# Performance work log

Hardware: AMD Instinct MI355X
Metric: run time of the kernel (lower is better)

## Reference

```python
import jax, jax.numpy as jnp
import numpy as np

D_MODEL = 2048
N_HEADS = 16
HEAD_DIM = D_MODEL // N_HEADS  # 128
B, T = 2, 2048


def setup_inputs() -> dict:
    key = jax.random.key(0)
    ks = jax.random.split(key, 9)
    s = 0.02
    x = jax.random.normal(ks[0], (B, T, D_MODEL), dtype=jnp.float32)
    # Per-head projection weights (stacked over heads); torch Linear y = x @ W^T + b,
    # here W is stored as [H, d_model, head_dim] so y = einsum('btc,hcd->bhtd').
    Wq = jax.random.normal(ks[1], (N_HEADS, D_MODEL, HEAD_DIM), dtype=jnp.float32) * s
    bq = jax.random.normal(ks[2], (N_HEADS, HEAD_DIM), dtype=jnp.float32) * s
    Wk = jax.random.normal(ks[3], (N_HEADS, D_MODEL, HEAD_DIM), dtype=jnp.float32) * s
    bk = jax.random.normal(ks[4], (N_HEADS, HEAD_DIM), dtype=jnp.float32) * s
    Wv = jax.random.normal(ks[5], (N_HEADS, D_MODEL, HEAD_DIM), dtype=jnp.float32) * s
    bv = jax.random.normal(ks[6], (N_HEADS, HEAD_DIM), dtype=jnp.float32) * s
    Wo = jax.random.normal(ks[7], (D_MODEL, D_MODEL), dtype=jnp.float32) * s  # used as y @ Wo
    bo = jax.random.normal(ks[8], (D_MODEL,), dtype=jnp.float32) * s
    return {"x": x, "Wq": Wq, "bq": bq, "Wk": Wk, "bk": bk,
            "Wv": Wv, "bv": bv, "Wo": Wo, "bo": bo}


def reference(x, Wq, bq, Wk, bk, Wv, bv, Wo, bo):
    # x: [B, T, C]; per-head Q/K/V projections -> [B, H, T, D]
    Bn, Tn, C = x.shape
    H, _, D = Wq.shape
    scale = D ** (-0.5)
    q = jnp.einsum('btc,hcd->bhtd', x, Wq) + bq[None, :, None, :]
    k = jnp.einsum('btc,hcd->bhtd', x, Wk) + bk[None, :, None, :]
    v = jnp.einsum('btc,hcd->bhtd', x, Wv) + bv[None, :, None, :]
    # scores [B, H, T, T] with additive causal mask (finfo.min above the diagonal)
    scores = jnp.einsum('bhtd,bhsd->bhts', q, k) * scale
    neg = jnp.finfo(scores.dtype).min
    causal = jnp.triu(jnp.full((Tn, Tn), neg, dtype=scores.dtype), k=1)
    probs = jax.nn.softmax(scores + causal, axis=-1)
    y = jnp.einsum('bhts,bhsd->bhtd', probs, v)  # [B, H, T, D]
    # concat heads along feature dim (head order preserved) then output projection
    y = y.transpose(0, 2, 1, 3).reshape(Bn, Tn, H * D)
    return y @ Wo + bo
```

## Files before the change

kernel.cpp:

```cpp
#include <hip/hip_runtime.h>
#include <stdint.h>

typedef unsigned short u16;
typedef __attribute__((ext_vector_type(4))) u16 u16x4;
typedef __attribute__((ext_vector_type(8))) u16 u16x8;
typedef __attribute__((ext_vector_type(8))) __bf16 bf16x8;
typedef __attribute__((ext_vector_type(4))) float f32x4;
typedef __attribute__((ext_vector_type(16))) float f32x16;

#define D_MODEL 2048
#define N_HEADS 16
#define HEAD_DIM 128
#define BATCH 2
#define SEQ 2048
#define M_TOT (BATCH*SEQ)
#define N_QKV (3*D_MODEL)

__device__ __forceinline__ u16 f2b(float f) {
  union { float f; uint32_t u; } c; c.f = f;
  uint32_t u = c.u;
  uint32_t r = (u + 0x7fffu + ((u >> 16) & 1u)) >> 16;
  return (u16)r;
}

__device__ __forceinline__ void gl_lds16(const u16* g, u16* l) {
  __builtin_amdgcn_global_load_lds(
      (const __attribute__((address_space(1))) uint32_t*)g,
      (__attribute__((address_space(3))) uint32_t*)l, 16, 0, 0);
}

template <int N> __device__ __forceinline__ void waitvm() {
  if constexpr (N == 6)      asm volatile("s_waitcnt vmcnt(6)" ::: "memory");
  else if constexpr (N == 5) asm volatile("s_waitcnt vmcnt(5)" ::: "memory");
  else                       asm volatile("s_waitcnt vmcnt(0)" ::: "memory");
}

__global__ __launch_bounds__(256) void prep_kernel(
    const float* __restrict__ x, u16* __restrict__ xb,
    const float* __restrict__ Wq, const float* __restrict__ Wk,
    const float* __restrict__ Wv, u16* __restrict__ Wt) {
  __shared__ u16 Tl[128][72];
  const int bid = blockIdx.x, tid = threadIdx.x;
  if (bid < 8192) {
    int i = (bid * 256 + tid) * 4;
    f32x4 v = *(const f32x4*)(x + i);
    u16x4 o;
    o[0] = f2b(v[0]); o[1] = f2b(v[1]); o[2] = f2b(v[2]); o[3] = f2b(v[3]);
    *(u16x4*)(xb + i) = o;
    return;
  }
  const int rel = bid - 8192;
  const int k0 = (rel & 31) * 64;
  const int hh = rel >> 5;
  const int qkv = hh >> 4, h = hh & 15;
  const float* src = (qkv == 0 ? Wq : qkv == 1 ? Wk : Wv) + (size_t)h * 2048 * 128;
  for (int it = 0; it < 32; ++it) {
    int idx = it * 256 + tid;
    int k = idx >> 7, d = idx & 127;
    Tl[d][k] = f2b(src[(size_t)(k0 + k) * 128 + d]);
  }
  __syncthreads();
  for (int it = 0; it < 32; ++it) {
    int idx = it * 256 + tid;
    int d = idx >> 6, kk = idx & 63;
    Wt[(size_t)(hh * 128 + d) * 2048 + k0 + kk] = Tl[d][kk];
  }
}

__global__ void trans_wo_kernel(const float* __restrict__ Wo, u16* __restrict__ Wot) {
  __shared__ u16 Tl[128][72];
  const int k0 = blockIdx.x * 64;
  const int n0 = blockIdx.y * 128;
  const int tid = threadIdx.x;
  for (int it = 0; it < 32; ++it) {
    int idx = it * 256 + tid;
    int k = idx >> 7, n = idx & 127;
    Tl[n][k] = f2b(Wo[(size_t)(k0 + k) * 2048 + n0 + n]);
  }
  __syncthreads();
  for (int it = 0; it < 32; ++it) {
    int idx = it * 256 + tid;
    int d = idx >> 6, kk = idx & 63;
    Wot[(size_t)(n0 + d) * 2048 + k0 + kk] = Tl[d][kk];
  }
}

__global__ void transpose_v_kernel(const u16* __restrict__ vb, u16* __restrict__ vt) {
  __shared__ u16 Tl[128 * 65];
  const int bh = blockIdx.y;
  const int t0 = blockIdx.x * 64;
  const int tid = threadIdx.x;
  const u16* src = vb + (size_t)bh * 2048 * 128;
  u16* dstp = vt + (size_t)bh * 128 * 2048;
#pragma unroll
  for (int c = 0; c < 4; ++c) {
    int ci = c * 256 + tid;
    int tr = ci >> 4, d0 = (ci & 15) * 8;
    u16x8 v = *(const u16x8*)(src + (size_t)(t0 + tr) * 128 + d0);
#pragma unroll
    for (int e = 0; e < 8; ++e) Tl[(d0 + e) * 65 + tr] = v[e];
  }
  __syncthreads();
#pragma unroll
  for (int it = 0; it < 32; ++it) {
    int idx = it * 256 + tid;
    int d = idx >> 6, tt = idx & 63;
    dstp[(size_t)d * 2048 + t0 + ((tt & 15) * 4 + (tt >> 4))] = Tl[d * 65 + tt];
  }
}

__global__ __launch_bounds__(512, 2) void gemm_qkv_kernel(
    const u16* __restrict__ A, const u16* __restrict__ B,
    u16* __restrict__ qo, u16* __restrict__ ko, u16* __restrict__ vo,
    const float* __restrict__ bq, const float* __restrict__ bk, const float* __restrict__ bv) {
  __shared__ u16 LS[3][20480];
  const int bid0 = blockIdx.x;
  const int gid = (bid0 & 7) * 32 + (bid0 >> 3);
  const int G = gid >> 4, l = gid & 15;
  const int m0 = ((G & 3) * 4 + (l & 3)) * 256;
  const int n0 = ((G >> 2) * 4 + (l >> 2)) * 384;

  const int tid = threadIdx.x, lane = tid & 63, w = tid >> 6;
  const int wm = (w >> 2) * 128, wn = (w & 3) * 96;
  const int l31 = lane & 31, g2 = lane >> 5;

  int aoff[2], boff[3];
#pragma unroll
  for (int l2 = 0; l2 < 2; ++l2) {
    int ci = l2 * 512 + tid, t = ci >> 3, x = (ci & 7) ^ (t & 7);
    aoff[l2] = (m0 + 2 * t + (x >> 2)) * 2048 + (x & 3) * 8;
  }
#pragma unroll
  for (int l2 = 0; l2 < 3; ++l2) {
    int ci = l2 * 512 + tid, t = ci >> 3, x = (ci & 7) ^ (t & 7);
    boff[l2] = (n0 + 2 * t + (x >> 2)) * 2048 + (x & 3) * 8;
  }
  const int adl = tid * 8;
  const int bdl = 8192 + tid * 8;

  f32x16 acc[4][3];
#pragma unroll
  for (int ai = 0; ai < 4; ++ai)
#pragma unroll
    for (int bj = 0; bj < 3; ++bj)
#pragma unroll
      for (int e = 0; e < 16; ++e) acc[ai][bj][e] = 0.f;

#pragma unroll
  for (int t = 0; t < 2; ++t) {
#pragma unroll
    for (int l2 = 0; l2 < 2; ++l2) gl_lds16(A + aoff[l2] + t * 32, LS[t] + adl + l2 * 4096);
#pragma unroll
    for (int l2 = 0; l2 < 3; ++l2) gl_lds16(B + boff[l2] + t * 32, LS[t] + bdl + l2 * 4096);
  }
  waitvm<5>();
  __builtin_amdgcn_s_barrier();

  int s = 0;
  for (int kt = 0; kt < 64; ++kt) {
    if (kt < 62) {
      const int s2 = (s == 0) ? 2 : s - 1;
      const int k2 = (kt + 2) * 32;
#pragma unroll
      for (int l2 = 0; l2 < 2; ++l2) gl_lds16(A + aoff[l2] + k2, LS[s2] + adl + l2 * 4096);
#pragma unroll
      for (int l2 = 0; l2 < 3; ++l2) gl_lds16(B + boff[l2] + k2, LS[s2] + bdl + l2 * 4096);
    }
    const char* base = (const char*)LS[s];
#pragma unroll
    for (int kk = 0; kk < 2; ++kk) {
      bf16x8 af[4];
#pragma unroll
      for (int ai = 0; ai < 4; ++ai) {
        int r = wm + ai * 32 + l31;
        int x = ((r & 1) << 2) | (2 * kk + g2);
        af[ai] = *(const bf16x8*)(base + (r >> 1) * 128 + 16 * (x ^ ((r >> 1) & 7)));
      }
      __builtin_amdgcn_s_setprio(1);
#pragma unroll
      for (int bj = 0; bj < 3; ++bj) {
        int rb = wn + bj * 32 + l31;
        int xb2 = ((rb & 1) << 2) | (2 * kk + g2);
        bf16x8 bfr = *(const bf16x8*)(base + 16384 + (rb >> 1) * 128 + 16 * (xb2 ^ ((rb >> 1) & 7)));
#pragma unroll
        for (int ai = 0; ai < 4; ++ai)
          acc[ai][bj] = __builtin_amdgcn_mfma_f32_32x32x16_bf16(af[ai], bfr, acc[ai][bj], 0, 0, 0);
      }
      __builtin_amdgcn_s_setprio(0);
    }
    if (kt < 62)       waitvm<5>();
    else if (kt == 62) waitvm<0>();
    __builtin_amdgcn_s_barrier();
    s = (s == 2) ? 0 : s + 1;
  }

  const float qscale = 0.08838834764831845f * 1.4426950408889634f;
#pragma unroll
  for (int bj = 0; bj < 3; ++bj) {
    const int n = n0 + wn + bj * 32 + l31;
    const int qkv = n >> 11, hh = (n >> 7) & 15, d = n & 127;
    const float* bias = (qkv == 0) ? bq : (qkv == 1) ? bk : bv;
    u16* dst = (qkv == 0) ? qo : (qkv == 1) ? ko : vo;
    const float bv_ = bias[n & 2047];
#pragma unroll
    for (int ai = 0; ai < 4; ++ai)
#pragma unroll
      for (int e = 0; e < 16; ++e) {
        int row = (e & 3) + 8 * (e >> 2) + 4 * g2;
        int gm = m0 + wm + ai * 32 + row;
        float val = acc[ai][bj][e] + bv_;
        if (qkv == 0) val *= qscale;
        int b = gm >> 11, t = gm & 2047;
        dst[((size_t)(b * 16 + hh) * 2048 + t) * 128 + d] = f2b(val);
      }
  }
}

__global__ __launch_bounds__(512, 2) void gemm_out_kernel(
    const u16* __restrict__ A, const u16* __restrict__ B,
    float* __restrict__ outf, const float* __restrict__ bo) {
  __shared__ u16 LS[3][24576];
  const int bid0 = blockIdx.x;
  const int gid = (bid0 & 7) * 32 + (bid0 >> 3);
  const int G = gid >> 4, l = gid & 15;
  const int m0 = ((G & 3) * 4 + (l & 3)) * 256;
  const int n0 = ((G >> 2) * 4 + (l >> 2)) * 128;

  const int tid = threadIdx.x, lane = tid & 63, w = tid >> 6;
  const int wm = (w >> 1) * 64, wn = (w & 1) * 64;
  const int lr = lane & 15, g = lane >> 4;
  const int kx = (lr & 7) << 4;

  int aoff[4], boff[2];
#pragma unroll
  for (int l2 = 0; l2 < 4; ++l2) {
    int ci = l2 * 512 + tid, r = ci >> 3, gj = ci & 7;
    aoff[l2] = (m0 + r) * 2048 + (gj ^ (r & 7)) * 8;
  }
#pragma unroll
  for (int l2 = 0; l2 < 2; ++l2) {
    int ci = l2 * 512 + tid, r = ci >> 3, gj = ci & 7;
    boff[l2] = (n0 + r) * 2048 + (gj ^ (r & 7)) * 8;
  }
  const int adl = tid * 8;
  const int bdl = 16384 + tid * 8;

  f32x4 acc[4][4];
  const f32x4 zero = {0.f, 0.f, 0.f, 0.f};
#pragma unroll
  for (int ai = 0; ai < 4; ++ai)
#pragma unroll
    for (int bj = 0; bj < 4; ++bj) acc[ai][bj] = zero;

#pragma unroll
  for (int t = 0; t < 2; ++t) {
#pragma unroll
    for (int l2 = 0; l2 < 4; ++l2) gl_lds16(A + aoff[l2] + t * 64, LS[t] + adl + l2 * 4096);
#pragma unroll
    for (int l2 = 0; l2 < 2; ++l2) gl_lds16(B + boff[l2] + t * 64, LS[t] + bdl + l2 * 4096);
  }
  waitvm<6>();
  __builtin_amdgcn_s_barrier();

  int s = 0;
  for (int kt = 0; kt < 32; ++kt) {
    if (kt < 30) {
      const int s2 = (s == 0) ? 2 : s - 1;
      const int k2 = (kt + 2) * 64;
#pragma unroll
      for (int l2 = 0; l2 < 4; ++l2) gl_lds16(A + aoff[l2] + k2, LS[s2] + adl + l2 * 4096);
#pragma unroll
      for (int l2 = 0; l2 < 2; ++l2) gl_lds16(B + boff[l2] + k2, LS[s2] + bdl + l2 * 4096);
    }
    const char* base = (const char*)LS[s];
#pragma unroll
    for (int h = 0; h < 2; ++h) {
      bf16x8 af[4];
#pragma unroll
      for (int ai = 0; ai < 4; ++ai) {
        int r = wm + ai * 16 + lr;
        af[ai] = *(const bf16x8*)(base + r * 128 + ((h * 64 + 16 * g) ^ kx));
      }
      __builtin_amdgcn_s_setprio(1);
#pragma unroll
      for (int bj = 0; bj < 4; ++bj) {
        int rb = wn + bj * 16 + lr;
        bf16x8 bfr = *(const bf16x8*)(base + 32768 + rb * 128 + ((h * 64 + 16 * g) ^ kx));
#pragma unroll
        for (int ai = 0; ai < 4; ++ai)
          acc[ai][bj] = __builtin_amdgcn_mfma_f32_16x16x32_bf16(af[ai], bfr, acc[ai][bj], 0, 0, 0);
      }
      __builtin_amdgcn_s_setprio(0);
    }
    if (kt < 30)       waitvm<6>();
    else if (kt == 30) waitvm<0>();
    __builtin_amdgcn_s_barrier();
    s = (s == 2) ? 0 : s + 1;
  }

  const int rbase = g * 4;
#pragma unroll
  for (int bj = 0; bj < 4; ++bj) {
    const int gn = n0 + wn + bj * 16 + lr;
    const float bv_ = bo[gn];
#pragma unroll
    for (int ai = 0; ai < 4; ++ai)
#pragma unroll
      for (int r = 0; r < 4; ++r) {
        int gm = m0 + wm + ai * 16 + rbase + r;
        outf[(size_t)gm * 2048 + gn] = acc[ai][bj][r] + bv_;
      }
  }
}

__global__ __launch_bounds__(256) void attn_kernel(
    const u16* __restrict__ qg, const u16* __restrict__ kg,
    const u16* __restrict__ vtg, u16* __restrict__ y) {
  __shared__ u16 Kb[2][64 * 128];
  __shared__ u16 Vb[2][128 * 64];
  __shared__ u16 Pl[4][32 * 64];
  const int tid = threadIdx.x, lane = tid & 63, w = tid >> 6;
  const int bid = blockIdx.x;
  const int bh = bid & 31, qt = 15 - (bid >> 5);
  const int b = bh >> 4, h = bh & 15;
  const int lr = lane & 15, lk = (lane >> 4) * 8;
  const u16* Qp = qg + (size_t)bh * (2048 * 128);
  const u16* Kp = kg + (size_t)bh * (2048 * 128);
  const u16* Vp = vtg + (size_t)bh * (128 * 2048);

  int koff[4], voff[4], dstc[4];
#pragma unroll
  for (int c = 0; c < 4; ++c) {
    int ci = c * 256 + tid;
    dstc[c] = ci * 8;
    int kr = ci >> 4, kj = ci & 15;
    koff[c] = kr * 128 + (kj ^ (kr & 7)) * 8;
    int vd = ci >> 3, vj = ci & 7;
    voff[c] = vd * 2048 + (vj ^ (vd & 7)) * 8;
  }
  const int kxor = (lr & 7) << 4;
  const int rbase = (lane >> 4) * 4;
  const f32x4 zero = {0.f, 0.f, 0.f, 0.f};

  const int q0 = qt * 128;
  const int qw = q0 + w * 32;
  const int nt = 2 * qt + 2;

  bf16x8 qf[2][4];
#pragma unroll
  for (int s = 0; s < 2; ++s)
#pragma unroll
    for (int i = 0; i < 4; ++i)
      qf[s][i] = *(const bf16x8*)(Qp + (size_t)(qw + s * 16 + lr) * 128 + i * 32 + lk);

  f32x4 o[2][8];
#pragma unroll
  for (int s = 0; s < 2; ++s)
#pragma unroll
    for (int f = 0; f < 8; ++f) o[s][f] = zero;
  float mrow[2][4], lrow[2][4];
#pragma unroll
  for (int s = 0; s < 2; ++s)
#pragma unroll
    for (int r = 0; r < 4; ++r) { mrow[s][r] = -1e30f; lrow[s][r] = 0.f; }

#pragma unroll
  for (int c = 0; c < 4; ++c) gl_lds16(Kp + koff[c], Kb[0] + dstc[c]);
#pragma unroll
  for (int c = 0; c < 4; ++c) gl_lds16(Vp + voff[c], Vb[0] + dstc[c]);
  __syncthreads();

  int cur = 0;
  for (int t = 0; t < nt; ++t) {
    const int s0 = t * 64;
    if (t + 1 < nt) {
      const size_t skn = (size_t)(s0 + 64) * 128;
#pragma unroll
      for (int c = 0; c < 4; ++c) gl_lds16(Kp + skn + koff[c], Kb[cur ^ 1] + dstc[c]);
#pragma unroll
      for (int c = 0; c < 4; ++c) gl_lds16(Vp + (s0 + 64) + voff[c], Vb[cur ^ 1] + dstc[c]);
    }
    if (s0 <= qw + 31) {
      const char* Kc = (const char*)Kb[cur];
      f32x4 sf[2][4];
      __builtin_amdgcn_s_setprio(1);
#pragma unroll
      for (int sj = 0; sj < 4; ++sj) {
        f32x4 a0 = zero, a1 = zero;
#pragma unroll
        for (int i = 0; i < 4; ++i) {
          bf16x8 kf = *(const bf16x8*)(Kc + ((((sj * 16 + lr) * 256) + (i * 32 + lk) * 2) ^ kxor));
          a0 = __builtin_amdgcn_mfma_f32_16x16x32_bf16(qf[0][i], kf, a0, 0, 0, 0);
          a1 = __builtin_amdgcn_mfma_f32_16x16x32_bf16(qf[1][i], kf, a1, 0, 0, 0);
        }
        sf[0][sj] = a0; sf[1][sj] = a1;
      }
      __builtin_amdgcn_s_setprio(0);

      char* Pc = (char*)Pl[w];
      const bool diag = (s0 + 63 > qw);
      float pmax[2][4];
      bool need = false;
#pragma unroll
      for (int s = 0; s < 2; ++s)
#pragma unroll
        for (int r = 0; r < 4; ++r) {
          if (diag) {
            const int rq = qw + s * 16 + rbase + r;
#pragma unroll
            for (int sj = 0; sj < 4; ++sj)
              if (s0 + sj * 16 + lr > rq) sf[s][sj][r] = -1e30f;
          }
          float pm = fmaxf(fmaxf(sf[s][0][r], sf[s][1][r]),
                           fmaxf(sf[s][2][r], sf[s][3][r]));
          pmax[s][r] = pm;
          need |= (pm > mrow[s][r] + 8.f);
        }
      if (__any(need)) {
#pragma unroll
        for (int s = 0; s < 2; ++s)
#pragma unroll
          for (int r = 0; r < 4; ++r) {
            float pm = pmax[s][r];
            pm = fmaxf(pm, __shfl_xor(pm, 1));
            pm = fmaxf(pm, __shfl_xor(pm, 2));
            pm = fmaxf(pm, __shfl_xor(pm, 4));
            pm = fmaxf(pm, __shfl_xor(pm, 8));
            float mnew = fmaxf(mrow[s][r], pm);
            float sfac = __builtin_amdgcn_exp2f(mrow[s][r] - mnew);
            mrow[s][r] = mnew;
            lrow[s][r] *= sfac;
#pragma unroll
            for (int f = 0; f < 8; ++f) o[s][f][r] *= sfac;
          }
      }
#pragma unroll
      for (int s = 0; s < 2; ++s)
#pragma unroll
        for (int r = 0; r < 4; ++r) {
          const int prow = s * 16 + rbase + r;
          float p0 = __builtin_amdgcn_exp2f(sf[s][0][r] - mrow[s][r]);
          float p1 = __builtin_amdgcn_exp2f(sf[s][1][r] - mrow[s][r]);
          float p2 = __builtin_amdgcn_exp2f(sf[s][2][r] - mrow[s][r]);
          float p3 = __builtin_amdgcn_exp2f(sf[s][3][r] - mrow[s][r]);
          lrow[s][r] += (p0 + p1) + (p2 + p3);
          uint32_t lo, hi;
          asm("v_cvt_pk_bf16_f32 %0, %1, %2" : "=v"(lo) : "v"(p0), "v"(p1));
          asm("v_cvt_pk_bf16_f32 %0, %1, %2" : "=v"(hi) : "v"(p2), "v"(p3));
          uint32_t* pp = (uint32_t*)(Pc + ((prow * 128 + lr * 8) ^ ((prow & 7) << 4)));
          pp[0] = lo; pp[1] = hi;
        }

      const char* Vc = (const char*)Vb[cur];
      __builtin_amdgcn_s_setprio(1);
#pragma unroll
      for (int st = 0; st < 2; ++st) {
        bf16x8 pf0 = *(const bf16x8*)(Pc + (((lr * 128) + (st * 32 + lk) * 2) ^ kxor));
        bf16x8 pf1 = *(const bf16x8*)(Pc + ((((16 + lr) * 128) + (st * 32 + lk) * 2) ^ kxor));
#pragma unroll
        for (int f = 0; f < 8; ++f) {
          bf16x8 vf = *(const bf16x8*)(Vc + ((((f * 16 + lr) * 128) + (st * 32 + lk) * 2) ^ kxor));
          o[0][f] = __builtin_amdgcn_mfma_f32_16x16x32_bf16(pf0, vf, o[0][f], 0, 0, 0);
          o[1][f] = __builtin_amdgcn_mfma_f32_16x16x32_bf16(pf1, vf, o[1][f], 0, 0, 0);
        }
      }
      __builtin_amdgcn_s_setprio(0);
    }
    __syncthreads();
    cur ^= 1;
  }

#pragma unroll
  for (int s = 0; s < 2; ++s)
#pragma unroll
    for (int r = 0; r < 4; ++r) {
      float l = lrow[s][r];
      l += __shfl_xor(l, 1);
      l += __shfl_xor(l, 2);
      l += __shfl_xor(l, 4);
      l += __shfl_xor(l, 8);
      const float rinv = __builtin_amdgcn_rcpf(l);
      const int row = qw + s * 16 + rbase + r;
#pragma unroll
      for (int f = 0; f < 8; ++f)
        y[((size_t)b * 2048 + row) * 2048 + h * 128 + f * 16 + lr] =
            f2b(o[s][f][r] * rinv);
    }
}


extern "C" void kernel_launch(void* const* d_in, const int* in_sizes, int n_in,
                              void* d_out, int out_size, void* d_ws, size_t ws_size,
                              hipStream_t stream) {
  const float* x  = (const float*)d_in[0];
  const float* Wq = (const float*)d_in[1];
  const float* bq = (const float*)d_in[2];
  const float* Wk = (const float*)d_in[3];
  const float* bk = (const float*)d_in[4];
  const float* Wv = (const float*)d_in[5];
  const float* bv = (const float*)d_in[6];
  const float* Wo = (const float*)d_in[7];
  const float* bo = (const float*)d_in[8];
  float* out = (float*)d_out;
  char* ws = (char*)d_ws;

  u16* xb  = (u16*)(ws + 0);
  u16* Wt  = (u16*)(ws + 16777216);
  u16* qb  = (u16*)(ws + 41943040);
  u16* kb  = (u16*)(ws + 58720256);
  u16* vb  = (u16*)(ws + 75497472);
  u16* Wot = Wt;
  u16* vtb = (u16*)(ws + 25165824);
  u16* yb  = xb;

  prep_kernel<<<9728, 256, 0, stream>>>(x, xb, Wq, Wk, Wv, Wt);
  gemm_qkv_kernel<<<256, 512, 0, stream>>>(xb, Wt, qb, kb, vb, bq, bk, bv);
  trans_wo_kernel<<<dim3(32, 16), 256, 0, stream>>>(Wo, Wot);
  transpose_v_kernel<<<dim3(32, 32), 256, 0, stream>>>(vb, vtb);
  attn_kernel<<<512, 256, 0, stream>>>(qb, kb, vtb, yb);
  gemm_out_kernel<<<256, 512, 0, stream>>>(yb, Wot, out, bo);
}
```

Measured before the change: 274.2 us.

## Fuse fp32-to-bf16 conversion of x into QKV GEMM loads and merge transposes

The QKV GEMM now loads fp32 x directly through registers, converts it to bf16 with packed cvt instructions and writes it to LDS one stage ahead. This removes the separate x conversion pass and its bf16 round trip through memory. The Wo and V transpose kernels are merged into one launch to cut launch overhead. In exchange the A operand no longer uses async global-to-LDS loads, so register pressure and the wait/barrier handling in the GEMM main loop change, which could reduce overlap.

```diff
diff --git a/kernel.cpp b/kernel.cpp
--- a/kernel.cpp
+++ b/kernel.cpp
@@ -2,8 +2,10 @@
 #include <stdint.h>
 
 typedef unsigned short u16;
+typedef unsigned int u32;
 typedef __attribute__((ext_vector_type(4))) u16 u16x4;
 typedef __attribute__((ext_vector_type(8))) u16 u16x8;
+typedef __attribute__((ext_vector_type(4))) u32 u32x4;
 typedef __attribute__((ext_vector_type(8))) __bf16 bf16x8;
 typedef __attribute__((ext_vector_type(4))) float f32x4;
 typedef __attribute__((ext_vector_type(16))) float f32x16;
@@ -30,28 +32,27 @@
 }
 
 template <int N> __device__ __forceinline__ void waitvm() {
-  if constexpr (N == 6)      asm volatile("s_waitcnt vmcnt(6)" ::: "memory");
+  if constexpr (N == 7)      asm volatile("s_waitcnt vmcnt(7)" ::: "memory");
+  else if constexpr (N == 6) asm volatile("s_waitcnt vmcnt(6)" ::: "memory");
   else if constexpr (N == 5) asm volatile("s_waitcnt vmcnt(5)" ::: "memory");
   else                       asm volatile("s_waitcnt vmcnt(0)" ::: "memory");
 }
+__device__ __forceinline__ void lgkm0() {
+  asm volatile("s_waitcnt lgkmcnt(0)" ::: "memory");
+}
+__device__ __forceinline__ u32 cvtpk(float a, float b) {
+  u32 r;
+  asm("v_cvt_pk_bf16_f32 %0, %1, %2" : "=v"(r) : "v"(a), "v"(b));
+  return r;
+}
 
 __global__ __launch_bounds__(256) void prep_kernel(
-    const float* __restrict__ x, u16* __restrict__ xb,
     const float* __restrict__ Wq, const float* __restrict__ Wk,
     const float* __restrict__ Wv, u16* __restrict__ Wt) {
   __shared__ u16 Tl[128][72];
   const int bid = blockIdx.x, tid = threadIdx.x;
-  if (bid < 8192) {
-    int i = (bid * 256 + tid) * 4;
-    f32x4 v = *(const f32x4*)(x + i);
-    u16x4 o;
-    o[0] = f2b(v[0]); o[1] = f2b(v[1]); o[2] = f2b(v[2]); o[3] = f2b(v[3]);
-    *(u16x4*)(xb + i) = o;
-    return;
-  }
-  const int rel = bid - 8192;
-  const int k0 = (rel & 31) * 64;
-  const int hh = rel >> 5;
+  const int k0 = (bid & 31) * 64;
+  const int hh = bid >> 5;
   const int qkv = hh >> 4, h = hh & 15;
   const float* src = (qkv == 0 ? Wq : qkv == 1 ? Wk : Wv) + (size_t)h * 2048 * 128;
   for (int it = 0; it < 32; ++it) {
@@ -67,29 +68,30 @@
   }
 }
 
-__global__ void trans_wo_kernel(const float* __restrict__ Wo, u16* __restrict__ Wot) {
-  __shared__ u16 Tl[128][72];
-  const int k0 = blockIdx.x * 64;
-  const int n0 = blockIdx.y * 128;
-  const int tid = threadIdx.x;
-  for (int it = 0; it < 32; ++it) {
-    int idx = it * 256 + tid;
-    int k = idx >> 7, n = idx & 127;
-    Tl[n][k] = f2b(Wo[(size_t)(k0 + k) * 2048 + n0 + n]);
-  }
-  __syncthreads();
-  for (int it = 0; it < 32; ++it) {
-    int idx = it * 256 + tid;
-    int d = idx >> 6, kk = idx & 63;
-    Wot[(size_t)(n0 + d) * 2048 + k0 + kk] = Tl[d][kk];
-  }
-}
-
-__global__ void transpose_v_kernel(const u16* __restrict__ vb, u16* __restrict__ vt) {
-  __shared__ u16 Tl[128 * 65];
-  const int bh = blockIdx.y;
-  const int t0 = blockIdx.x * 64;
-  const int tid = threadIdx.x;
+__global__ __launch_bounds__(256) void post_transpose_kernel(
+    const float* __restrict__ Wo, u16* __restrict__ Wot,
+    const u16* __restrict__ vb, u16* __restrict__ vt) {
+  __shared__ u16 Tl[128 * 72];
+  const int bid = blockIdx.x, tid = threadIdx.x;
+  if (bid < 512) {
+    const int k0 = (bid & 31) * 64;
+    const int n0 = (bid >> 5) * 128;
+    for (int it = 0; it < 32; ++it) {
+      int idx = it * 256 + tid;
+      int k = idx >> 7, n = idx & 127;
+      Tl[n * 72 + k] = f2b(Wo[(size_t)(k0 + k) * 2048 + n0 + n]);
+    }
+    __syncthreads();
+    for (int it = 0; it < 32; ++it) {
+      int idx = it * 256 + tid;
+      int d = idx >> 6, kk = idx & 63;
+      Wot[(size_t)(n0 + d) * 2048 + k0 + kk] = Tl[d * 72 + kk];
+    }
+    return;
+  }
+  const int rel = bid - 512;
+  const int t0 = (rel & 31) * 64;
+  const int bh = rel >> 5;
   const u16* src = vb + (size_t)bh * 2048 * 128;
   u16* dstp = vt + (size_t)bh * 128 * 2048;
 #pragma unroll
@@ -98,19 +100,19 @@
     int tr = ci >> 4, d0 = (ci & 15) * 8;
     u16x8 v = *(const u16x8*)(src + (size_t)(t0 + tr) * 128 + d0);
 #pragma unroll
-    for (int e = 0; e < 8; ++e) Tl[(d0 + e) * 65 + tr] = v[e];
+    for (int e = 0; e < 8; ++e) Tl[(d0 + e) * 72 + tr] = v[e];
   }
   __syncthreads();
 #pragma unroll
   for (int it = 0; it < 32; ++it) {
     int idx = it * 256 + tid;
     int d = idx >> 6, tt = idx & 63;
-    dstp[(size_t)d * 2048 + t0 + ((tt & 15) * 4 + (tt >> 4))] = Tl[d * 65 + tt];
+    dstp[(size_t)d * 2048 + t0 + ((tt & 15) * 4 + (tt >> 4))] = Tl[d * 72 + tt];
   }
 }
 
 __global__ __launch_bounds__(512, 2) void gemm_qkv_kernel(
-    const u16* __restrict__ A, const u16* __restrict__ B,
+    const float* __restrict__ X, const u16* __restrict__ B,
     u16* __restrict__ qo, u16* __restrict__ ko, u16* __restrict__ vo,
     const float* __restrict__ bq, const float* __restrict__ bk, const float* __restrict__ bv) {
   __shared__ u16 LS[3][20480];
@@ -146,25 +148,52 @@
 #pragma unroll
       for (int e = 0; e < 16; ++e) acc[ai][bj][e] = 0.f;
 
-#pragma unroll
-  for (int t = 0; t < 2; ++t) {
-#pragma unroll
-    for (int l2 = 0; l2 < 2; ++l2) gl_lds16(A + aoff[l2] + t * 32, LS[t] + adl + l2 * 4096);
-#pragma unroll
-    for (int l2 = 0; l2 < 3; ++l2) gl_lds16(B + boff[l2] + t * 32, LS[t] + bdl + l2 * 4096);
+  f32x4 t0a = *(const f32x4*)(X + aoff[0]);
+  f32x4 t0b = *(const f32x4*)(X + aoff[0] + 4);
+  f32x4 t1a = *(const f32x4*)(X + aoff[1]);
+  f32x4 t1b = *(const f32x4*)(X + aoff[1] + 4);
+  f32x4 rc0a = *(const f32x4*)(X + aoff[0] + 32);
+  f32x4 rc0b = *(const f32x4*)(X + aoff[0] + 36);
+  f32x4 rc1a = *(const f32x4*)(X + aoff[1] + 32);
+  f32x4 rc1b = *(const f32x4*)(X + aoff[1] + 36);
+#pragma unroll
+  for (int t = 0; t < 2; ++t)
+#pragma unroll
+    for (int l2 = 0; l2 < 3; ++l2)
+      gl_lds16(B + boff[l2] + t * 32, LS[t] + bdl + l2 * 4096);
+  {
+    u32x4 w0 = {cvtpk(t0a[0], t0a[1]), cvtpk(t0a[2], t0a[3]),
+                cvtpk(t0b[0], t0b[1]), cvtpk(t0b[2], t0b[3])};
+    u32x4 w1 = {cvtpk(t1a[0], t1a[1]), cvtpk(t1a[2], t1a[3]),
+                cvtpk(t1b[0], t1b[1]), cvtpk(t1b[2], t1b[3])};
+    *(__shared__ u32x4*)(LS[0] + adl) = w0;
+    *(__shared__ u32x4*)(LS[0] + adl + 4096) = w1;
   }
   waitvm<5>();
+  lgkm0();
   __builtin_amdgcn_s_barrier();
 
   int s = 0;
   for (int kt = 0; kt < 64; ++kt) {
+    const int sw = (s == 2) ? 0 : s + 1;
+    f32x4 rn0a, rn0b, rn1a, rn1b;
     if (kt < 62) {
       const int s2 = (s == 0) ? 2 : s - 1;
       const int k2 = (kt + 2) * 32;
-#pragma unroll
-      for (int l2 = 0; l2 < 2; ++l2) gl_lds16(A + aoff[l2] + k2, LS[s2] + adl + l2 * 4096);
+      rn0a = *(const f32x4*)(X + aoff[0] + k2);
+      rn0b = *(const f32x4*)(X + aoff[0] + k2 + 4);
+      rn1a = *(const f32x4*)(X + aoff[1] + k2);
+      rn1b = *(const f32x4*)(X + aoff[1] + k2 + 4);
 #pragma unroll
       for (int l2 = 0; l2 < 3; ++l2) gl_lds16(B + boff[l2] + k2, LS[s2] + bdl + l2 * 4096);
+    }
+    if (kt < 63) {
+      u32x4 w0 = {cvtpk(rc0a[0], rc0a[1]), cvtpk(rc0a[2], rc0a[3]),
+                  cvtpk(rc0b[0], rc0b[1]), cvtpk(rc0b[2], rc0b[3])};
+      u32x4 w1 = {cvtpk(rc1a[0], rc1a[1]), cvtpk(rc1a[2], rc1a[3]),
+                  cvtpk(rc1b[0], rc1b[1]), cvtpk(rc1b[2], rc1b[3])};
+      *(__shared__ u32x4*)(LS[sw] + adl) = w0;
+      *(__shared__ u32x4*)(LS[sw] + adl + 4096) = w1;
     }
     const char* base = (const char*)LS[s];
 #pragma unroll
@@ -188,10 +217,12 @@
       }
       __builtin_amdgcn_s_setprio(0);
     }
-    if (kt < 62)       waitvm<5>();
+    if (kt < 62)       waitvm<7>();
     else if (kt == 62) waitvm<0>();
+    lgkm0();
     __builtin_amdgcn_s_barrier();
-    s = (s == 2) ? 0 : s + 1;
+    rc0a = rn0a; rc0b = rn0b; rc1a = rn1a; rc1b = rn1b;
+    s = sw;
   }
 
   const float qscale = 0.08838834764831845f * 1.4426950408889634f;
@@ -444,9 +475,7 @@
           float p2 = __builtin_amdgcn_exp2f(sf[s][2][r] - mrow[s][r]);
           float p3 = __builtin_amdgcn_exp2f(sf[s][3][r] - mrow[s][r]);
           lrow[s][r] += (p0 + p1) + (p2 + p3);
-          uint32_t lo, hi;
-          asm("v_cvt_pk_bf16_f32 %0, %1, %2" : "=v"(lo) : "v"(p0), "v"(p1));
-          asm("v_cvt_pk_bf16_f32 %0, %1, %2" : "=v"(hi) : "v"(p2), "v"(p3));
+          uint32_t lo = cvtpk(p0, p1), hi = cvtpk(p2, p3);
           uint32_t* pp = (uint32_t*)(Pc + ((prow * 128 + lr * 8) ^ ((prow & 7) << 4)));
           pp[0] = lo; pp[1] = hi;
         }
@@ -504,19 +533,17 @@
   float* out = (float*)d_out;
   char* ws = (char*)d_ws;
 
-  u16* xb  = (u16*)(ws + 0);
+  u16* yb  = (u16*)(ws + 0);
   u16* Wt  = (u16*)(ws + 16777216);
   u16* qb  = (u16*)(ws + 41943040);
   u16* kb  = (u16*)(ws + 58720256);
   u16* vb  = (u16*)(ws + 75497472);
   u16* Wot = Wt;
   u16* vtb = (u16*)(ws + 25165824);
-  u16* yb  = xb;
-
-  prep_kernel<<<9728, 256, 0, stream>>>(x, xb, Wq, Wk, Wv, Wt);
-  gemm_qkv_kernel<<<256, 512, 0, stream>>>(xb, Wt, qb, kb, vb, bq, bk, bv);
-  trans_wo_kernel<<<dim3(32, 16), 256, 0, stream>>>(Wo, Wot);
-  transpose_v_kernel<<<dim3(32, 32), 256, 0, stream>>>(vb, vtb);
+
+  prep_kernel<<<1536, 256, 0, stream>>>(Wq, Wk, Wv, Wt);
+  gemm_qkv_kernel<<<256, 512, 0, stream>>>(x, Wt, qb, kb, vb, bq, bk, bv);
+  post_transpose_kernel<<<1536, 256, 0, stream>>>(Wo, Wot, vb, vtb);
   attn_kernel<<<512, 256, 0, stream>>>(qb, kb, vtb, yb);
   gemm_out_kernel<<<256, 512, 0, stream>>>(yb, Wot, out, bo);
 }
```

New measurement: 263.6 us (median of 3 runs). 1.04x faster.
